# Optimization experiments

Hardware: AMD Instinct MI355X
Metric: run time of the kernel (lower is better)

The kernel has to match this reference:

```python
import jax, jax.numpy as jnp
import numpy as np

# bin sizes: logspace(-3,0,20) seconds, keep those < (t_end - t_start)/2 = 0.25 s, in ms
_bs = np.logspace(-3, 0, 20)
BIN_MS = [int(b) for b in np.round(_bs[_bs < 0.25] * 1000).astype(int)]  # 16 bins: [1,1,2,3,4,6,9,13,18,26,38,55,78,113,162,234]

SYNC_COST = 10.0
T_START_MS, T_END_MS = 0, 500
EPS = 1e-7


def setup_inputs() -> dict:
    C, B, T, N, N_E = 50, 8, 600, 30000, 24000
    rng = np.random.default_rng(42)
    spikes = (rng.random((B, T, N)) < 0.02).astype(np.float32)
    sample_trials = rng.integers(0, B, size=C).astype(np.int32)
    # sample_counts ~ N(70, 30) clipped to [15, N_E], consecutive chunks of a shuffled e-id list
    counts = np.clip(rng.normal(70.0, 30.0, C).astype(np.int64), 15, N_E)
    e_ids = rng.permutation(N_E)
    sel_mask = np.zeros((C, N), dtype=bool)
    prev = 0
    for i in range(C):
        cn = int(counts[i])
        if prev + cn > N_E:
            e_ids = rng.permutation(e_ids)
            prev = 0
        sel_mask[i, e_ids[prev:prev + cn]] = True
        prev += cn
    exp_fanos = (rng.random(len(BIN_MS)) * 1.5 + 0.5).astype(np.float32)
    return {
        "spikes": jnp.asarray(spikes),
        "exp_fanos": jnp.asarray(exp_fanos),
        "sample_trials": jnp.asarray(sample_trials),
        "sel_mask": jnp.asarray(sel_mask),
    }


def reference(spikes, exp_fanos, sample_trials, sel_mask):
    # trim to analysis window: [B, 500, N]
    sp = spikes[:, T_START_MS:T_END_MS, :]
    C = sel_mask.shape[0]
    m = sel_mask.astype(sp.dtype)  # [C, N]
    # population spike count per sample: sum over selected e-cells.
    # M[b, t, c] = sum_n sp[b,t,n] * m[c,n]; then pick the sampled trial per c.
    M = jnp.einsum('btn,cn->btc', sp, m)                 # [B, T, C] (small)
    selected = M[sample_trials, :, jnp.arange(C)]        # [C, T]
    T = selected.shape[1]
    fanos = []
    for b in BIN_MS:  # fixed small set of bin sizes
        nb = T // b
        # conv1d(ones, stride=b, VALID) == non-overlapping binned sums
        counts = selected[:, :nb * b].reshape(C, nb, b).sum(axis=-1)  # [C, nb]
        mean_count = jnp.maximum(counts.mean(axis=1), EPS)
        var_count = counts.var(axis=1)  # population variance, matches tf.math.reduce_variance
        fanos.append(jnp.mean(var_count / mean_count))
    fanos = jnp.stack(fanos)  # [16]
    mse_loss = jnp.mean(jnp.square(exp_fanos - fanos))
    return SYNC_COST * mse_loss
```

## Files before the change

### kernel.cpp

```cpp
#include <hip/hip_runtime.h>

#define C_CLS 50
#define B_TR 8
#define T_FULL 600
#define T_USE 500
#define N_NEU 30000
#define CAP 1024
#define NBINS 16
#define EPS 1e-7

__device__ __constant__ int d_bins[NBINS] = {1,1,2,3,4,6,9,13,18,26,38,55,78,113,162,234};

__global__ void init_flags_kernel(int* flags) {
    if (threadIdx.x < 8) flags[threadIdx.x] = 0;
}

__global__ void detect_mode_kernel(const unsigned int* __restrict__ w, int* flags) {
    const int nwords = C_CLS * N_NEU / 4;
    int stride = gridDim.x * blockDim.x;
    int fF = 0, fB = 0, fO = 0, fD = 0;
    for (int i = blockIdx.x * blockDim.x + threadIdx.x; i < nwords; i += stride) {
        unsigned int v = w[i];
        if (v == 0u) continue;
        if (v == 0x3F800000u) fF = 1;
        else if (v == 0x3FF00000u && (i & 1)) fD = 1;
        else {
            unsigned int b0 = v & 0xFFu, b1 = (v >> 8) & 0xFFu,
                         b2 = (v >> 16) & 0xFFu, b3 = (v >> 24) & 0xFFu;
            bool byteOK = (b0 <= 1u) && (b1 <= 1u) && (b2 <= 1u) && (b3 <= 1u);
            if (byteOK && v != 1u) fB = 1;
        }
        if (i & 1) fO = 1;
    }
    if (fF) atomicOr(&flags[0], 1);
    if (fB) atomicOr(&flags[1], 1);
    if (fO) atomicOr(&flags[2], 1);
    if (fD) atomicOr(&flags[3], 1);
}

__device__ __forceinline__ int mode_from_flags(const int* flags) {
    if (flags[0]) return 2;
    if (flags[3]) return 4;
    if (flags[1]) return 1;
    if (flags[2]) return 0;
    return 3;
}

__global__ void build_lists_kernel(const void* mask, const int* flags,
                                   int* cnt, int* idx) {
    int c = blockIdx.x;
    __shared__ int sc;
    __shared__ int smode;
    if (threadIdx.x == 0) { sc = 0; smode = mode_from_flags(flags); }
    __syncthreads();
    int mode = smode;
    for (int n = threadIdx.x; n < N_NEU; n += blockDim.x) {
        long long e = (long long)c * N_NEU + n;
        bool sel;
        switch (mode) {
            case 0:  sel = ((const int*)mask)[e] != 0; break;
            case 1:  sel = ((const unsigned char*)mask)[e] != 0; break;
            case 2:  sel = ((const float*)mask)[e] != 0.0f; break;
            case 3:  sel = ((const long long*)mask)[e] != 0LL; break;
            default: sel = ((const double*)mask)[e] != 0.0; break;
        }
        if (sel) {
            int p = atomicAdd(&sc, 1);
            if (p < CAP) idx[c * CAP + p] = n;
        }
    }
    __syncthreads();
    if (threadIdx.x == 0) cnt[c] = min(sc, CAP);
}

__global__ void gather_kernel(const float* __restrict__ spikes,
                              const int* __restrict__ trials,
                              const int* __restrict__ cnt,
                              const int* __restrict__ idx,
                              float* __restrict__ selected) {
    int c = blockIdx.x;
    __shared__ int sidx[CAP];
    int kn = cnt[c];
    for (int k = threadIdx.x; k < kn; k += blockDim.x) sidx[k] = idx[c * CAP + k];
    __syncthreads();
    int b = trials[c];
    int t = blockIdx.y * blockDim.x + threadIdx.x;
    if (t >= T_USE) return;
    const float* __restrict__ row =
        spikes + ((long long)b * T_FULL + t) * N_NEU;
    float s = 0.f;
    int k = 0;
    for (; k + 16 <= kn; k += 16) {
        float p = 0.f;
#pragma unroll
        for (int u = 0; u < 16; ++u) p += row[sidx[k + u]];
        s += p;
    }
    for (; k < kn; ++k) s += row[sidx[k]];
    selected[c * T_USE + t] = s;
}

__global__ void fano_kernel(const float* __restrict__ selected,
                            float* __restrict__ fanos) {
    int bin = blockIdx.x;
    int b = d_bins[bin];
    int nb = T_USE / b;
    int c = threadIdx.x;
    float fano = 0.f;
    if (c < C_CLS) {
        const float* row = selected + c * T_USE;
        double s1 = 0.0, s2 = 0.0;
        for (int i = 0; i < nb; ++i) {
            float cs = 0.f;
            int base = i * b;
            for (int j = 0; j < b; ++j) cs += row[base + j];
            s1 += cs;
            s2 += (double)cs * (double)cs;
        }
        double mean = s1 / nb;
        double var = s2 / nb - mean * mean;
        if (var < 0.0) var = 0.0;
        double m = mean > EPS ? mean : EPS;
        fano = (float)(var / m);
    }
    for (int off = 32; off > 0; off >>= 1) fano += __shfl_down(fano, off);
    if (threadIdx.x == 0) fanos[bin] = fano / (float)C_CLS;
}

__global__ void loss_kernel(const float* __restrict__ fanos,
                            const float* __restrict__ exp_fanos,
                            float* __restrict__ out) {
    int t = threadIdx.x;
    float sq = 0.f;
    if (t < NBINS) {
        float d = exp_fanos[t] - fanos[t];
        sq = d * d;
    }
    for (int off = 32; off > 0; off >>= 1) sq += __shfl_down(sq, off);
    if (t == 0) out[0] = 10.0f * sq / (float)NBINS;
}

extern "C" void kernel_launch(void* const* d_in, const int* in_sizes, int n_in,
                              void* d_out, int out_size, void* d_ws, size_t ws_size,
                              hipStream_t stream) {
    const float* spikes    = (const float*)d_in[0];
    const float* exp_fanos = (const float*)d_in[1];
    const int*   trials    = (const int*)d_in[2];
    const void*  mask      = d_in[3];
    float* out = (float*)d_out;

    char* ws = (char*)d_ws;
    int*   flags    = (int*)(ws + 0);
    int*   cnt      = (int*)(ws + 256);
    float* fanos    = (float*)(ws + 512);
    int*   idx      = (int*)(ws + 1024);
    float* selected = (float*)(ws + 1024 + (size_t)C_CLS * CAP * 4);

    init_flags_kernel<<<1, 64, 0, stream>>>(flags);
    detect_mode_kernel<<<512, 256, 0, stream>>>((const unsigned int*)mask, flags);
    build_lists_kernel<<<C_CLS, 256, 0, stream>>>(mask, flags, cnt, idx);
    gather_kernel<<<dim3(C_CLS, 8), 64, 0, stream>>>(spikes, trials, cnt, idx, selected);
    fano_kernel<<<NBINS, 64, 0, stream>>>(selected, fanos);
    loss_kernel<<<1, 64, 0, stream>>>(fanos, exp_fanos, out);
}
```

Before: 169.9 us.

## Split gather over neuron slices with atomic accumulation and padded index list

The gather kernel now launches eight times as many blocks, each handling a strided slice of the selected-neuron list, and merges partial sums with atomicAdd into a zero-initialized output. The index list is padded so each 16-wide unrolled batch of loads is issued unconditionally and masked by multiplication, giving more memory-level parallelism. The aim is more in-flight scattered loads and better GPU occupancy for a latency-bound gather, at the cost of float atomics, which make summation order nondeterministic, and an extra zeroing pass.

```diff
diff --git a/kernel.cpp b/kernel.cpp
--- a/kernel.cpp
+++ b/kernel.cpp
@@ -7,12 +7,15 @@
 #define N_NEU 30000
 #define CAP 1024
 #define NBINS 16
+#define NSLICE 8
 #define EPS 1e-7
 
 __device__ __constant__ int d_bins[NBINS] = {1,1,2,3,4,6,9,13,18,26,38,55,78,113,162,234};
 
-__global__ void init_flags_kernel(int* flags) {
-    if (threadIdx.x < 8) flags[threadIdx.x] = 0;
+__global__ void init_kernel(int* flags, float* selected) {
+    int i = blockIdx.x * blockDim.x + threadIdx.x;
+    if (i < 8) flags[i] = 0;
+    if (i < C_CLS * T_USE) selected[i] = 0.0f;
 }
 
 __global__ void detect_mode_kernel(const unsigned int* __restrict__ w, int* flags) {
@@ -79,25 +82,30 @@
                               const int* __restrict__ idx,
                               float* __restrict__ selected) {
     int c = blockIdx.x;
-    __shared__ int sidx[CAP];
+    __shared__ int sidx[CAP + 16 * NSLICE];
     int kn = cnt[c];
+    int pad = idx[c * CAP];
     for (int k = threadIdx.x; k < kn; k += blockDim.x) sidx[k] = idx[c * CAP + k];
+    for (int k = kn + threadIdx.x; k < kn + 16 * NSLICE; k += blockDim.x) sidx[k] = pad;
     __syncthreads();
     int b = trials[c];
     int t = blockIdx.y * blockDim.x + threadIdx.x;
     if (t >= T_USE) return;
+    int s = blockIdx.z;
     const float* __restrict__ row =
         spikes + ((long long)b * T_FULL + t) * N_NEU;
-    float s = 0.f;
-    int k = 0;
-    for (; k + 16 <= kn; k += 16) {
-        float p = 0.f;
+    float acc = 0.f;
+    for (int kk = s; kk < kn; kk += 16 * NSLICE) {
+        float v[16];
 #pragma unroll
-        for (int u = 0; u < 16; ++u) p += row[sidx[k + u]];
-        s += p;
+        for (int u = 0; u < 16; ++u) {
+            int k2 = kk + u * NSLICE;
+            v[u] = row[sidx[k2]] * ((k2 < kn) ? 1.0f : 0.0f);
+        }
+#pragma unroll
+        for (int u = 0; u < 16; ++u) acc += v[u];
     }
-    for (; k < kn; ++k) s += row[sidx[k]];
-    selected[c * T_USE + t] = s;
+    atomicAdd(&selected[c * T_USE + t], acc);
 }
 
 __global__ void fano_kernel(const float* __restrict__ selected,
@@ -156,10 +164,10 @@
     int*   idx      = (int*)(ws + 1024);
     float* selected = (float*)(ws + 1024 + (size_t)C_CLS * CAP * 4);
 
-    init_flags_kernel<<<1, 64, 0, stream>>>(flags);
+    init_kernel<<<(C_CLS * T_USE + 255) / 256, 256, 0, stream>>>(flags, selected);
     detect_mode_kernel<<<512, 256, 0, stream>>>((const unsigned int*)mask, flags);
     build_lists_kernel<<<C_CLS, 256, 0, stream>>>(mask, flags, cnt, idx);
-    gather_kernel<<<dim3(C_CLS, 8), 64, 0, stream>>>(spikes, trials, cnt, idx, selected);
+    gather_kernel<<<dim3(C_CLS, 8, NSLICE), 64, 0, stream>>>(spikes, trials, cnt, idx, selected);
     fano_kernel<<<NBINS, 64, 0, stream>>>(selected, fanos);
     loss_kernel<<<1, 64, 0, stream>>>(fanos, exp_fanos, out);
 }
```

New measurement: 169.6 us. About the same (-0.2%).

## Replace index gather with bitmask ballot-popcount streaming over spike rows

Applied to the files above, without the earlier changes.

Converts each class's selection mask into 64-bit ballot bitmasks and groups classes by sampled trial. Each (trial, time) row of spikes is then read once, coalesced, and turned into a wave ballot, and every class sharing that trial counts its selected spikes with popcount. This replaces the scattered per-class index gathers. It assumes spikes are binary (a nonzero value counts as one), assumes at most 64 classes per trial, and streams the full row even for classes with few selected neurons.

```diff
diff --git a/kernel.cpp b/kernel.cpp
--- a/kernel.cpp
+++ b/kernel.cpp
@@ -5,14 +5,17 @@
 #define T_FULL 600
 #define T_USE 500
 #define N_NEU 30000
-#define CAP 1024
+#define NG 469
+#define BSTRIDE 472
 #define NBINS 16
 #define EPS 1e-7
 
 __device__ __constant__ int d_bins[NBINS] = {1,1,2,3,4,6,9,13,18,26,38,55,78,113,162,234};
 
-__global__ void init_flags_kernel(int* flags) {
-    if (threadIdx.x < 8) flags[threadIdx.x] = 0;
+
+__global__ void init_kernel(int* flags, int* ncls) {
+    int i = threadIdx.x;
+    if (i < 8) { flags[i] = 0; ncls[i] = 0; }
 }
 
 __global__ void detect_mode_kernel(const unsigned int* __restrict__ w, int* flags) {
@@ -46,58 +49,73 @@
     return 3;
 }
 
-__global__ void build_lists_kernel(const void* mask, const int* flags,
-                                   int* cnt, int* idx) {
+__global__ void build_bits_kernel(const void* mask, const int* flags,
+                                  unsigned long long* bits) {
     int c = blockIdx.x;
-    __shared__ int sc;
-    __shared__ int smode;
-    if (threadIdx.x == 0) { sc = 0; smode = mode_from_flags(flags); }
-    __syncthreads();
-    int mode = smode;
-    for (int n = threadIdx.x; n < N_NEU; n += blockDim.x) {
-        long long e = (long long)c * N_NEU + n;
-        bool sel;
-        switch (mode) {
-            case 0:  sel = ((const int*)mask)[e] != 0; break;
-            case 1:  sel = ((const unsigned char*)mask)[e] != 0; break;
-            case 2:  sel = ((const float*)mask)[e] != 0.0f; break;
-            case 3:  sel = ((const long long*)mask)[e] != 0LL; break;
-            default: sel = ((const double*)mask)[e] != 0.0; break;
+    int lane = threadIdx.x;
+    int mode = mode_from_flags(flags);
+    for (int g = blockIdx.y; g < NG; g += gridDim.y) {
+        int n = g * 64 + lane;
+        bool sel = false;
+        if (n < N_NEU) {
+            long long e = (long long)c * N_NEU + n;
+            switch (mode) {
+                case 0:  sel = ((const int*)mask)[e] != 0; break;
+                case 1:  sel = ((const unsigned char*)mask)[e] != 0; break;
+                case 2:  sel = ((const float*)mask)[e] != 0.0f; break;
+                case 3:  sel = ((const long long*)mask)[e] != 0LL; break;
+                default: sel = ((const double*)mask)[e] != 0.0; break;
+            }
         }
-        if (sel) {
-            int p = atomicAdd(&sc, 1);
-            if (p < CAP) idx[c * CAP + p] = n;
-        }
+        unsigned long long w = __ballot(sel);
+        if (lane == 0) bits[(long long)c * BSTRIDE + g] = w;
     }
-    __syncthreads();
-    if (threadIdx.x == 0) cnt[c] = min(sc, CAP);
 }
 
-__global__ void gather_kernel(const float* __restrict__ spikes,
-                              const int* __restrict__ trials,
-                              const int* __restrict__ cnt,
-                              const int* __restrict__ idx,
-                              float* __restrict__ selected) {
-    int c = blockIdx.x;
-    __shared__ int sidx[CAP];
-    int kn = cnt[c];
-    for (int k = threadIdx.x; k < kn; k += blockDim.x) sidx[k] = idx[c * CAP + k];
+__global__ void trial_cls_kernel(const int* __restrict__ trials,
+                                 int* ncls, int* cls_of_trial) {
+    int c = threadIdx.x;
+    if (c < C_CLS) {
+        int b = trials[c];
+        int p = atomicAdd(&ncls[b], 1);
+        cls_of_trial[b * 64 + p] = c;
+    }
+}
+
+__global__ void __launch_bounds__(256)
+stream_kernel(const float* __restrict__ spikes,
+              const int* __restrict__ ncls,
+              const int* __restrict__ cls_of_trial,
+              const unsigned long long* __restrict__ bits,
+              float* __restrict__ selected) {
+    int bt = blockIdx.x;
+    int b = bt / T_USE;
+    int t = bt - b * T_USE;
+    int nc = ncls[b];
+    if (nc == 0) return;
+    int lane = threadIdx.x & 63;
+    int wid = threadIdx.x >> 6;
+    int myc = cls_of_trial[b * 64 + (lane < nc ? lane : 0)];
+    const unsigned long long* __restrict__ bp = bits + (long long)myc * BSTRIDE;
+    const float* __restrict__ row = spikes + ((long long)b * T_FULL + t) * N_NEU;
+    int acc = 0;
+    int g0 = wid * 118;
+    int g1 = g0 + 118; if (g1 > NG) g1 = NG;
+#pragma unroll 4
+    for (int g = g0; g < g1; ++g) {
+        int n = g * 64 + lane;
+        int n2 = n < N_NEU ? n : N_NEU - 1;
+        float v = row[n2] * (n < N_NEU ? 1.0f : 0.0f);
+        unsigned long long bm = __ballot(v != 0.0f);
+        if (lane < nc) acc += __popcll(bm & bp[g]);
+    }
+    __shared__ int sacc[4][64];
+    sacc[wid][lane] = acc;
     __syncthreads();
-    int b = trials[c];
-    int t = blockIdx.y * blockDim.x + threadIdx.x;
-    if (t >= T_USE) return;
-    const float* __restrict__ row =
-        spikes + ((long long)b * T_FULL + t) * N_NEU;
-    float s = 0.f;
-    int k = 0;
-    for (; k + 16 <= kn; k += 16) {
-        float p = 0.f;
-#pragma unroll
-        for (int u = 0; u < 16; ++u) p += row[sidx[k + u]];
-        s += p;
+    if (wid == 0 && lane < nc) {
+        int s = sacc[0][lane] + sacc[1][lane] + sacc[2][lane] + sacc[3][lane];
+        selected[myc * T_USE + t] = (float)s;
     }
-    for (; k < kn; ++k) s += row[sidx[k]];
-    selected[c * T_USE + t] = s;
 }
 
 __global__ void fano_kernel(const float* __restrict__ selected,
@@ -150,16 +168,18 @@
     float* out = (float*)d_out;
 
     char* ws = (char*)d_ws;
-    int*   flags    = (int*)(ws + 0);
-    int*   cnt      = (int*)(ws + 256);
-    float* fanos    = (float*)(ws + 512);
-    int*   idx      = (int*)(ws + 1024);
-    float* selected = (float*)(ws + 1024 + (size_t)C_CLS * CAP * 4);
+    int*   flags   = (int*)(ws + 0);
+    int*   ncls    = (int*)(ws + 256);
+    int*   clsofb  = (int*)(ws + 512);
+    float* fanos   = (float*)(ws + 4096);
+    unsigned long long* bits = (unsigned long long*)(ws + 8192);
+    float* selected = (float*)(ws + 200704);
 
-    init_flags_kernel<<<1, 64, 0, stream>>>(flags);
+    init_kernel<<<1, 64, 0, stream>>>(flags, ncls);
     detect_mode_kernel<<<512, 256, 0, stream>>>((const unsigned int*)mask, flags);
-    build_lists_kernel<<<C_CLS, 256, 0, stream>>>(mask, flags, cnt, idx);
-    gather_kernel<<<dim3(C_CLS, 8), 64, 0, stream>>>(spikes, trials, cnt, idx, selected);
+    build_bits_kernel<<<dim3(C_CLS, 8), 64, 0, stream>>>(mask, flags, bits);
+    trial_cls_kernel<<<1, 64, 0, stream>>>(trials, ncls, clsofb);
+    stream_kernel<<<B_TR * T_USE, 256, 0, stream>>>(spikes, ncls, clsofb, bits, selected);
     fano_kernel<<<NBINS, 64, 0, stream>>>(selected, fanos);
     loss_kernel<<<1, 64, 0, stream>>>(fanos, exp_fanos, out);
 }
```

New measurement: 338.9 us. 1.99x slower.
